# Performance work log

Hardware: AMD Instinct MI355X
Metric: run time of the kernel (lower is better)

Reference implementation:

```python
import jax, jax.numpy as jnp
import numpy as np

N, E, F, C, ED, G, D = 50000, 1000000, 30, 64, 11, 1024, 256


def setup_inputs() -> dict:
    key = jax.random.key(0)
    ks = jax.random.split(key, 20)
    rn = lambda k, shape, s=0.1: jax.random.normal(k, shape, jnp.float32) * s
    return {
        "x": rn(ks[0], (N, F), 1.0),
        "edge_attr": jax.random.uniform(ks[1], (E, ED), jnp.float32),
        "W0": rn(ks[2], (F, C)), "asrc0": rn(ks[3], (C,)), "adst0": rn(ks[4], (C,)),
        "We0": rn(ks[5], (ED, C)), "ae0": rn(ks[6], (C,)), "Wres0": rn(ks[7], (F, C)),
        "b0": jnp.zeros((C,), jnp.float32),
        "W": rn(ks[8], (3, C, C)), "asrc": rn(ks[9], (3, C)), "adst": rn(ks[10], (3, C)),
        "We": rn(ks[11], (3, ED, C)), "ae": rn(ks[12], (3, C)), "Wres": rn(ks[13], (3, C, C)),
        "b": jnp.zeros((3, C), jnp.float32),
        "Wout": rn(ks[14], (2 * C, D)), "bout": jnp.zeros((D,), jnp.float32),
        "edge_index": jax.random.randint(ks[15], (2, E), 0, N),
        "batch_index": jnp.sort(jax.random.randint(ks[16], (N,), 0, G)),
    }


def _gat(x, src, dst, edge_attr, W, asrc, adst, We, ae, Wres, b):
    """PyG GATConv (heads=1) with edge_dim and residual=True."""
    n = x.shape[0]
    h = x @ W                                   # [N, C]
    e = edge_attr @ We                          # [E, C]
    alpha = (jnp.sum(h * asrc, -1)[src]
             + jnp.sum(h * adst, -1)[dst]
             + jnp.sum(e * ae, -1))             # [E]
    alpha = jax.nn.leaky_relu(alpha, 0.2)
    m = jax.ops.segment_max(alpha, dst, num_segments=n)
    a = jnp.exp(alpha - m[dst])
    s = jax.ops.segment_sum(a, dst, num_segments=n)
    a = a / (s[dst] + 1e-16)                    # per-dst softmax
    out = jax.ops.segment_sum(a[:, None] * h[src], dst, num_segments=n)
    return out + x @ Wres + b


def reference(x, edge_attr, W0, asrc0, adst0, We0, ae0, Wres0, b0,
              W, asrc, adst, We, ae, Wres, b, Wout, bout,
              edge_index, batch_index):
    src, dst = edge_index[0], edge_index[1]
    h = jax.nn.leaky_relu(
        _gat(x, src, dst, edge_attr, W0, asrc0, adst0, We0, ae0, Wres0, b0), 0.01)
    for i in range(3):  # conv1..conv3 (fixed small layer loop)
        h = _gat(h, src, dst, edge_attr, W[i], asrc[i], adst[i],
                 We[i], ae[i], Wres[i], b[i])
        if i < 2:
            h = jax.nn.leaky_relu(h, 0.01)
    gmax = jax.ops.segment_max(h, batch_index, num_segments=G)
    gmax = jnp.where(jnp.isfinite(gmax), gmax, 0.0)  # empty graphs -> 0
    cnt = jax.ops.segment_sum(jnp.ones((h.shape[0],), h.dtype), batch_index,
                              num_segments=G)
    gmean = jax.ops.segment_sum(h, batch_index, num_segments=G) / jnp.maximum(cnt, 1.0)[:, None]
    pooled = jax.nn.leaky_relu(jnp.concatenate([gmax, gmean], axis=1), 0.01)
    return pooled @ Wout + bout
```

## Files before the change

### kernel.cpp

```cpp
#include <hip/hip_runtime.h>
#include <hip/hip_fp16.h>

#define NN 50000
#define NE 1000000
#define FIN0 30
#define C 64
#define ED 11
#define NG 1024
#define DOUT 256
#define NBIN 196
#define PA_EDGES 1024

typedef unsigned long long ull;

__global__ __launch_bounds__(256) void hist196_kernel(const int* __restrict__ dst,
    int* __restrict__ bcnt){
  __shared__ int h[256];
  int t=threadIdx.x;
  h[t]=0;
  __syncthreads();
  for(int i=blockIdx.x*256+t;i<NE;i+=gridDim.x*256)
    atomicAdd(&h[dst[i]>>8],1);
  __syncthreads();
  if(h[t]) atomicAdd(&bcnt[t],h[t]);
}

__global__ __launch_bounds__(256) void scan196_kernel(const int* __restrict__ bcnt,
    int* __restrict__ bbase, int* __restrict__ gcur){
  __shared__ int p[256];
  int t=threadIdx.x;
  int v=bcnt[t];
  p[t]=v; __syncthreads();
  #pragma unroll
  for(int off=1;off<256;off<<=1){
    int u=(t>=off)?p[t-off]:0;
    __syncthreads(); p[t]+=u; __syncthreads();
  }
  int ex=p[t]-v;
  if(t<=NBIN) bbase[t]=ex;
  if(t<NBIN)  gcur[t]=ex;
}

__global__ __launch_bounds__(256) void grow_kernel(const int* __restrict__ batch,
    int* __restrict__ growptr){
  int i=blockIdx.x*256+threadIdx.x;
  if(i>=NN) return;
  int bi=batch[i];
  int bp=(i==0)?-1:batch[i-1];
  for(int g=bp+1;g<=bi;++g) growptr[g]=i;
  if(i==NN-1){ for(int g=bi+1;g<=NG;++g) growptr[g]=NN; }
}

__global__ __launch_bounds__(256) void part_kernel(const int* __restrict__ dst,
    const int* __restrict__ src, const float* __restrict__ edge_attr,
    const float* __restrict__ We0, const float* __restrict__ ae0,
    const float* __restrict__ We,  const float* __restrict__ ae,
    int* __restrict__ gcur,
    ull* __restrict__ pdst_src, ushort4* __restrict__ ped){
  __shared__ ull     ldst_src[PA_EDGES];
  __shared__ ushort4 led[PA_EDGES];
  __shared__ unsigned char lbin[PA_EDGES];
  __shared__ float tile[256*ED];
  __shared__ float sw[4][ED];
  __shared__ int hist[256], p[256], sc[256], lofs[256], bb[256];
  int t=threadIdx.x;
  hist[t]=0;
  if(t<4*ED){
    int l=t/ED, j=t%ED;
    const float* wp=(l==0)? (We0+(size_t)j*C) : (We+((size_t)(l-1)*ED+j)*C);
    const float* ap=(l==0)? ae0 : (ae+(size_t)(l-1)*C);
    float s=0.f;
    for(int c=0;c<C;++c) s+=wp[c]*ap[c];
    sw[l][j]=s;
  }
  __syncthreads();
  size_t e0=(size_t)blockIdx.x*PA_EDGES;
  int cnt=(int)min((size_t)PA_EDGES,(size_t)NE-e0);
  for(int i=t;i<cnt;i+=256) atomicAdd(&hist[dst[e0+i]>>8],1);
  __syncthreads();
  p[t]=hist[t]; __syncthreads();
  #pragma unroll
  for(int off=1;off<256;off<<=1){
    int u=(t>=off)?p[t-off]:0;
    __syncthreads(); p[t]+=u; __syncthreads();
  }
  sc[t]=p[t]-hist[t];
  lofs[t]=sc[t];
  bb[t]=(hist[t]>0)?atomicAdd(&gcur[t],hist[t]):0;
  __syncthreads();
  for(int base=0;base<cnt;base+=256){
    int ccnt=min(256,cnt-base);
    for(int i=t;i<ccnt*ED;i+=256) tile[i]=edge_attr[(e0+base)*ED+i];
    __syncthreads();
    if(t<ccnt){
      int i=base+t;
      int d=dst[e0+i], s=src[e0+i];
      int b=d>>8;
      float d0=0,d1=0,d2=0,d3=0;
      #pragma unroll
      for(int j=0;j<ED;++j){
        float ev=tile[t*ED+j];
        d0=fmaf(ev,sw[0][j],d0);
        d1=fmaf(ev,sw[1][j],d1);
        d2=fmaf(ev,sw[2][j],d2);
        d3=fmaf(ev,sw[3][j],d3);
      }
      int slot=atomicAdd(&lofs[b],1);
      ldst_src[slot]=((ull)(unsigned)d<<32)|(unsigned)s;
      ushort4 hv;
      hv.x=__half_as_ushort(__float2half(d0));
      hv.y=__half_as_ushort(__float2half(d1));
      hv.z=__half_as_ushort(__float2half(d2));
      hv.w=__half_as_ushort(__float2half(d3));
      led[slot]=hv;
      lbin[slot]=(unsigned char)b;
    }
    __syncthreads();
  }
  for(int i=t;i<cnt;i+=256){
    int b=lbin[i];
    int g=bb[b]+i-sc[b];
    pdst_src[g]=ldst_src[i];
    ped[g]=led[i];
  }
}

__global__ __launch_bounds__(256) void build_kernel(const ull* __restrict__ pdst_src,
    const ushort4* __restrict__ ped, const int* __restrict__ bbase,
    int* __restrict__ rowptr, int* __restrict__ src_csr, ushort* __restrict__ edch){
  __shared__ int cnt[256], p[256], cur[256];
  int t=threadIdx.x, b=blockIdx.x;
  int n0=b<<8;
  cnt[t]=0;
  __syncthreads();
  int beg=bbase[b], endd=bbase[b+1];
  for(int j=beg+t;j<endd;j+=256)
    atomicAdd(&cnt[(int)(pdst_src[j]>>32)-n0],1);
  __syncthreads();
  int v=cnt[t];
  p[t]=v; __syncthreads();
  #pragma unroll
  for(int off=1;off<256;off<<=1){
    int u=(t>=off)?p[t-off]:0;
    __syncthreads(); p[t]+=u; __syncthreads();
  }
  int ex=p[t]-v;
  cur[t]=beg+ex;
  if(n0+t<NN) rowptr[n0+t]=beg+ex;
  if(b==0&&t==0) rowptr[NN]=NE;
  __syncthreads();
  for(int j=beg+t;j<endd;j+=256){
    ull ds=pdst_src[j];
    int d=(int)(ds>>32);
    int s=(int)(ds&0xffffffffu);
    int pos=atomicAdd(&cur[d-n0],1);
    src_csr[pos]=s;
    ushort4 e=ped[j];
    edch[pos]=e.x;
    edch[(size_t)NE+pos]=e.y;
    edch[2*(size_t)NE+pos]=e.z;
    edch[3*(size_t)NE+pos]=e.w;
  }
}

template<int FIN, int SXS>
__global__ __launch_bounds__(256) void feat_kernel(const float* __restrict__ in,
    const float* __restrict__ W, const float* __restrict__ Wres,
    const float* __restrict__ bvec, const float* __restrict__ av_src,
    const float* __restrict__ av_dst,
    __half* __restrict__ hW16, float* __restrict__ outb,
    float* __restrict__ as_, float* __restrict__ ad_){
  __shared__ float sW[FIN*C], sR[FIN*C];
  __shared__ float sx[64*SXS];
  __shared__ float sb[C], ss[C], sd[C];
  int tid=threadIdx.x;
  if(tid<C){ sb[tid]=bvec[tid]; ss[tid]=av_src[tid]; sd[tid]=av_dst[tid]; }
  for(int i=tid;i<FIN*C;i+=256){ sW[i]=W[i]; sR[i]=Wres[i]; }
  int nbase=blockIdx.x*64;
  int nvalid=min(64,NN-nbase);
  if constexpr (FIN==64){
    const float4* in4=(const float4*)(in+(size_t)nbase*64);
    for(int i=tid;i<1024;i+=256){
      int n=i>>4, k=(i&15)*4;
      float4 v=(n<nvalid)?in4[i]:make_float4(0.f,0.f,0.f,0.f);
      *(float4*)&sx[n*SXS+k]=v;
    }
  } else {
    for(int i=tid;i<64*FIN;i+=256){
      int n=i/FIN, k=i-n*FIN;
      sx[n*SXS+k]=(n<nvalid)?in[(size_t)(nbase+n)*FIN+k]:0.f;
    }
  }
  __syncthreads();
  int w=tid>>6, lane=tid&63;
  int ng=lane>>4, cl=lane&15;
  int n0=w*16+ng*4;
  int c0=cl*4;
  float hw[4][4]={}, hr[4][4]={};
  const float* sxp=&sx[n0*SXS];
  #pragma unroll 2
  for(int k=0;k<FIN;k+=2){
    float4 wv0=*(const float4*)&sW[k*C+c0];
    float4 rv0=*(const float4*)&sR[k*C+c0];
    float4 wv1=*(const float4*)&sW[(k+1)*C+c0];
    float4 rv1=*(const float4*)&sR[(k+1)*C+c0];
    float2 x0=*(const float2*)&sxp[k];
    float2 x1=*(const float2*)&sxp[SXS+k];
    float2 x2=*(const float2*)&sxp[2*SXS+k];
    float2 x3=*(const float2*)&sxp[3*SXS+k];
    float xa[4]={x0.x,x1.x,x2.x,x3.x};
    float xb[4]={x0.y,x1.y,x2.y,x3.y};
    #pragma unroll
    for(int r=0;r<4;++r){
      hw[r][0]=fmaf(xa[r],wv0.x,hw[r][0]);
      hw[r][1]=fmaf(xa[r],wv0.y,hw[r][1]);
      hw[r][2]=fmaf(xa[r],wv0.z,hw[r][2]);
      hw[r][3]=fmaf(xa[r],wv0.w,hw[r][3]);
      hr[r][0]=fmaf(xa[r],rv0.x,hr[r][0]);
      hr[r][1]=fmaf(xa[r],rv0.y,hr[r][1]);
      hr[r][2]=fmaf(xa[r],rv0.z,hr[r][2]);
      hr[r][3]=fmaf(xa[r],rv0.w,hr[r][3]);
      hw[r][0]=fmaf(xb[r],wv1.x,hw[r][0]);
      hw[r][1]=fmaf(xb[r],wv1.y,hw[r][1]);
      hw[r][2]=fmaf(xb[r],wv1.z,hw[r][2]);
      hw[r][3]=fmaf(xb[r],wv1.w,hw[r][3]);
      hr[r][0]=fmaf(xb[r],rv1.x,hr[r][0]);
      hr[r][1]=fmaf(xb[r],rv1.y,hr[r][1]);
      hr[r][2]=fmaf(xb[r],rv1.z,hr[r][2]);
      hr[r][3]=fmaf(xb[r],rv1.w,hr[r][3]);
    }
  }
  float s0=ss[c0], s1=ss[c0+1], s2=ss[c0+2], s3=ss[c0+3];
  float d0=sd[c0], d1=sd[c0+1], d2=sd[c0+2], d3=sd[c0+3];
  float b0v=sb[c0], b1v=sb[c0+1], b2v=sb[c0+2], b3v=sb[c0+3];
  #pragma unroll
  for(int r=0;r<4;++r){
    int n=n0+r;
    float ps=hw[r][0]*s0+hw[r][1]*s1+hw[r][2]*s2+hw[r][3]*s3;
    float pd=hw[r][0]*d0+hw[r][1]*d1+hw[r][2]*d2+hw[r][3]*d3;
    #pragma unroll
    for(int off=1;off<16;off<<=1){ ps+=__shfl_xor(ps,off,64); pd+=__shfl_xor(pd,off,64); }
    if(n<nvalid){
      size_t gn=(size_t)(nbase+n);
      ushort4 hv;
      hv.x=__half_as_ushort(__float2half(hw[r][0]));
      hv.y=__half_as_ushort(__float2half(hw[r][1]));
      hv.z=__half_as_ushort(__float2half(hw[r][2]));
      hv.w=__half_as_ushort(__float2half(hw[r][3]));
      *(ushort4*)&hW16[gn*C+c0]=hv;
      float4 ov;
      ov.x=hr[r][0]+b0v; ov.y=hr[r][1]+b1v; ov.z=hr[r][2]+b2v; ov.w=hr[r][3]+b3v;
      *(float4*)&outb[gn*C+c0]=ov;
      if(cl==0){ as_[gn]=ps; ad_[gn]=pd; }
    }
  }
}

__device__ __forceinline__ void acc8(float* a, float at, uint4 u){
  __half2 h0=*(__half2*)&u.x, h1=*(__half2*)&u.y, h2=*(__half2*)&u.z, h3=*(__half2*)&u.w;
  float2 f0=__half22float2(h0), f1=__half22float2(h1);
  float2 f2=__half22float2(h2), f3=__half22float2(h3);
  a[0]=fmaf(at,f0.x,a[0]); a[1]=fmaf(at,f0.y,a[1]);
  a[2]=fmaf(at,f1.x,a[2]); a[3]=fmaf(at,f1.y,a[3]);
  a[4]=fmaf(at,f2.x,a[4]); a[5]=fmaf(at,f2.y,a[5]);
  a[6]=fmaf(at,f3.x,a[6]); a[7]=fmaf(at,f3.y,a[7]);
}

__global__ __launch_bounds__(256) void agg_kernel(const int* __restrict__ rowptr,
    const int* __restrict__ src_csr, const ushort* __restrict__ edc_l,
    const float* __restrict__ as_, const float* __restrict__ ad_,
    const __half* __restrict__ hW16, float* __restrict__ outb, int relu){
  __shared__ float2 sws[4][64];
  int w=threadIdx.x>>6, lane=threadIdx.x&63;
  int nidx=blockIdx.x*4+w;
  if(nidx>=NN) return;
  int beg=rowptr[nidx], end=rowptr[nidx+1];
  int deg=end-beg;
  float ad_n=ad_[nidx];
  int g2=lane>>3, gl2=lane&7;
  const uint4* hw4=(const uint4*)hW16;
  float s=0.f;
  float acc[8]={0.f,0.f,0.f,0.f,0.f,0.f,0.f,0.f};

  if(deg<=64){
    int j=beg+lane;
    float al=-INFINITY; int sl=0;
    if(lane<deg){
      sl=src_csr[j];
      float a=as_[sl]+ad_n+__half2float(__ushort_as_half(edc_l[j]));
      al=(a>0.f)?a:0.2f*a;
    }
    float mn=al;
    #pragma unroll
    for(int off=32;off;off>>=1) mn=fmaxf(mn,__shfl_xor(mn,off,64));
    float wl=(lane<deg)?__expf(al-mn):0.f;
    s=wl;
    #pragma unroll
    for(int off=32;off;off>>=1) s+=__shfl_xor(s,off,64);
    float2 pr; pr.x=wl; pr.y=__int_as_float(sl);
    sws[w][lane]=pr;
    int t=g2;
    for(; t+8<deg; t+=16){
      float2 r0=sws[w][t], r1=sws[w][t+8];
      uint4 u0=hw4[(size_t)__float_as_int(r0.y)*8+gl2];
      uint4 u1=hw4[(size_t)__float_as_int(r1.y)*8+gl2];
      acc8(acc,r0.x,u0);
      acc8(acc,r1.x,u1);
    }
    if(t<deg){
      float2 r=sws[w][t];
      uint4 u=hw4[(size_t)__float_as_int(r.y)*8+gl2];
      acc8(acc,r.x,u);
    }
  } else {
    float m=-INFINITY;
    for(int base=beg;base<end;base+=64){
      int j=base+lane;
      float al=-INFINITY; int sl=0;
      if(j<end){
        sl=src_csr[j];
        float a=as_[sl]+ad_n+__half2float(__ushort_as_half(edc_l[j]));
        al=(a>0.f)?a:0.2f*a;
      }
      float cm=al;
      #pragma unroll
      for(int off=32;off;off>>=1) cm=fmaxf(cm,__shfl_xor(cm,off,64));
      float mn=fmaxf(m,cm);
      float scale=(m==-INFINITY)?0.f:__expf(m-mn);
      s*=scale;
      #pragma unroll
      for(int i=0;i<8;++i) acc[i]*=scale;
      float wl=(j<end)?__expf(al-mn):0.f;
      float cs=wl;
      #pragma unroll
      for(int off=32;off;off>>=1) cs+=__shfl_xor(cs,off,64);
      s+=cs; m=mn;
      float2 pr; pr.x=wl; pr.y=__int_as_float(sl);
      sws[w][lane]=pr;
      int cnt=min(64,end-base);
      int t=g2;
      for(; t+8<cnt; t+=16){
        float2 r0=sws[w][t], r1=sws[w][t+8];
        uint4 u0=hw4[(size_t)__float_as_int(r0.y)*8+gl2];
        uint4 u1=hw4[(size_t)__float_as_int(r1.y)*8+gl2];
        acc8(acc,r0.x,u0);
        acc8(acc,r1.x,u1);
      }
      if(t<cnt){
        float2 r=sws[w][t];
        uint4 u=hw4[(size_t)__float_as_int(r.y)*8+gl2];
        acc8(acc,r.x,u);
      }
    }
  }

  #pragma unroll
  for(int off=8;off<64;off<<=1){
    #pragma unroll
    for(int i=0;i<8;++i) acc[i]+=__shfl_xor(acc[i],off,64);
  }
  if(g2==0){
    float denom=s+1e-16f;
    size_t o0=(size_t)nidx*C+gl2*8;
    float4 oa=*(float4*)&outb[o0];
    float4 ob=*(float4*)&outb[o0+4];
    float4 va,vb;
    va.x=acc[0]/denom+oa.x; va.y=acc[1]/denom+oa.y;
    va.z=acc[2]/denom+oa.z; va.w=acc[3]/denom+oa.w;
    vb.x=acc[4]/denom+ob.x; vb.y=acc[5]/denom+ob.y;
    vb.z=acc[6]/denom+ob.z; vb.w=acc[7]/denom+ob.w;
    if(relu){
      va.x=(va.x>0.f)?va.x:0.01f*va.x; va.y=(va.y>0.f)?va.y:0.01f*va.y;
      va.z=(va.z>0.f)?va.z:0.01f*va.z; va.w=(va.w>0.f)?va.w:0.01f*va.w;
      vb.x=(vb.x>0.f)?vb.x:0.01f*vb.x; vb.y=(vb.y>0.f)?vb.y:0.01f*vb.y;
      vb.z=(vb.z>0.f)?vb.z:0.01f*vb.z; vb.w=(vb.w>0.f)?vb.w:0.01f*vb.w;
    }
    *(float4*)&outb[o0]=va;
    *(float4*)&outb[o0+4]=vb;
  }
}

__global__ __launch_bounds__(256) void pool_kernel(const float* __restrict__ h,
    const int* __restrict__ growptr, float* __restrict__ pooled){
  int w=threadIdx.x>>6, lane=threadIdx.x&63;
  int g=blockIdx.x*4+w;
  if(g>=NG) return;
  int beg=growptr[g], end=growptr[g+1];
  float mx=-INFINITY, sm=0.f;
  for(int n=beg;n<end;++n){ float v=h[(size_t)n*C+lane]; mx=fmaxf(mx,v); sm+=v; }
  int cnt=end-beg;
  float gm=(cnt==0)?0.f:mx;
  float mean=sm/fmaxf((float)cnt,1.f);
  gm=(gm>0.f)?gm:0.01f*gm;
  mean=(mean>0.f)?mean:0.01f*mean;
  pooled[(size_t)g*128+lane]=gm;
  pooled[(size_t)g*128+64+lane]=mean;
}

__global__ __launch_bounds__(256) void out_kernel(const float* __restrict__ pooled,
    const float* __restrict__ Wout, const float* __restrict__ bout,
    float* __restrict__ out){
  __shared__ float sp[128];
  int g=blockIdx.x, d=threadIdx.x;
  if(d<128) sp[d]=pooled[(size_t)g*128+d];
  __syncthreads();
  float o=bout[d];
  for(int k=0;k<128;++k) o=fmaf(sp[k],Wout[k*DOUT+d],o);
  out[(size_t)g*DOUT+d]=o;
}

extern "C" void kernel_launch(void* const* d_in, const int* in_sizes, int n_in,
                              void* d_out, int out_size, void* d_ws, size_t ws_size,
                              hipStream_t stream){
  const float* x        =(const float*)d_in[0];
  const float* edge_attr=(const float*)d_in[1];
  const float* W0       =(const float*)d_in[2];
  const float* asrc0    =(const float*)d_in[3];
  const float* adst0    =(const float*)d_in[4];
  const float* We0      =(const float*)d_in[5];
  const float* ae0      =(const float*)d_in[6];
  const float* Wres0    =(const float*)d_in[7];
  const float* b0       =(const float*)d_in[8];
  const float* W        =(const float*)d_in[9];
  const float* asrc     =(const float*)d_in[10];
  const float* adst     =(const float*)d_in[11];
  const float* We       =(const float*)d_in[12];
  const float* ae       =(const float*)d_in[13];
  const float* Wres     =(const float*)d_in[14];
  const float* b        =(const float*)d_in[15];
  const float* Wout     =(const float*)d_in[16];
  const float* bout     =(const float*)d_in[17];
  const int* edge_index =(const int*)d_in[18];
  const int* batch_index=(const int*)d_in[19];
  const int* src=edge_index;
  const int* dst=edge_index+NE;

  char* p=(char*)d_ws;
  auto take=[&](size_t bytes)->void*{ void* r=(void*)p; p+=(bytes+255)&~(size_t)255; return r; };
  int* rowptr  =(int*)take((size_t)(NN+1)*4);
  int* growptr =(int*)take((size_t)(NG+1)*4);
  int* bcnt    =(int*)take((size_t)256*4);
  int* bbase   =(int*)take((size_t)256*4);
  int* gcur    =(int*)take((size_t)256*4);
  int* src_csr =(int*)take((size_t)NE*4);
  float* as_   =(float*)take((size_t)NN*4);
  float* ad_   =(float*)take((size_t)NN*4);
  ushort* edch =(ushort*)take((size_t)NE*4*2);
  __half* hW16 =(__half*)take((size_t)NN*C*2);
  float* bufA  =(float*)take((size_t)NN*C*4);
  ull* pdst_src=(ull*)take((size_t)NE*8);
  float* pooled=(float*)pdst_src;
  ushort4* ped =(ushort4*)take((size_t)NN*C*4);
  float* bufB  =(float*)ped;
  (void)ws_size; (void)in_sizes; (void)n_in; (void)out_size;

  hipMemsetAsync(bcnt,0,(size_t)256*4,stream);
  hist196_kernel<<<1024,256,0,stream>>>(dst,bcnt);
  scan196_kernel<<<1,256,0,stream>>>(bcnt,bbase,gcur);
  grow_kernel<<<(NN+255)/256,256,0,stream>>>(batch_index,growptr);

  part_kernel<<<(NE+PA_EDGES-1)/PA_EDGES,256,0,stream>>>(dst,src,edge_attr,
      We0,ae0,We,ae,gcur,pdst_src,ped);
  build_kernel<<<NBIN,256,0,stream>>>(pdst_src,ped,bbase,rowptr,src_csr,edch);

  const int nblkF=(NN+63)/64;
  const int nblkA=(NN+3)/4;
  feat_kernel<FIN0,36><<<nblkF,256,0,stream>>>(x,W0,Wres0,b0,asrc0,adst0,hW16,bufA,as_,ad_);
  agg_kernel<<<nblkA,256,0,stream>>>(rowptr,src_csr,edch,as_,ad_,hW16,bufA,1);
  float* bin=bufA; float* bo=bufB;
  for(int i=0;i<3;++i){
    feat_kernel<C,68><<<nblkF,256,0,stream>>>(bin,W+(size_t)i*C*C,Wres+(size_t)i*C*C,
        b+(size_t)i*C,asrc+(size_t)i*C,adst+(size_t)i*C,hW16,bo,as_,ad_);
    agg_kernel<<<nblkA,256,0,stream>>>(rowptr,src_csr,edch+(size_t)(i+1)*NE,as_,ad_,hW16,bo,(i<2)?1:0);
    float* t=bin; bin=bo; bo=t;
  }
  pool_kernel<<<(NG+3)/4,256,0,stream>>>(bin,growptr,pooled);
  out_kernel<<<NG,256,0,stream>>>(pooled,Wout,bout,(float*)d_out);
}
```

Before: 338.2 us.

## Process two nodes per wavefront in aggregation and pack partition records into uint4

The aggregation kernel now assigns two destination nodes per 64-lane wavefront, one per 32-lane half, when every degree in the wave is at most 32. Waves with a larger degree fall back to a sequential per-node loop. This targets idle lanes, since the average degree is about 20 and many lanes sat unused. The partition step also merges the dst/src and half-precision edge-score arrays into one 16-byte record and doubles the edges per partition block, giving fewer, wider stores and loads. The grid size NN/8 relies on NN being divisible by 8, and the fallback path serialises the two nodes.

```diff
diff --git a/kernel.cpp b/kernel.cpp
--- a/kernel.cpp
+++ b/kernel.cpp
@@ -9,7 +9,7 @@
 #define NG 1024
 #define DOUT 256
 #define NBIN 196
-#define PA_EDGES 1024
+#define PA_EDGES 2048
 
 typedef unsigned long long ull;
 
@@ -55,10 +55,8 @@
     const int* __restrict__ src, const float* __restrict__ edge_attr,
     const float* __restrict__ We0, const float* __restrict__ ae0,
     const float* __restrict__ We,  const float* __restrict__ ae,
-    int* __restrict__ gcur,
-    ull* __restrict__ pdst_src, ushort4* __restrict__ ped){
-  __shared__ ull     ldst_src[PA_EDGES];
-  __shared__ ushort4 led[PA_EDGES];
+    int* __restrict__ gcur, uint4* __restrict__ prec){
+  __shared__ uint4 lrec[PA_EDGES];
   __shared__ unsigned char lbin[PA_EDGES];
   __shared__ float tile[256*ED];
   __shared__ float sw[4][ED];
@@ -105,14 +103,14 @@
         d2=fmaf(ev,sw[2][j],d2);
         d3=fmaf(ev,sw[3][j],d3);
       }
+      uint4 r;
+      r.x=(unsigned)d; r.y=(unsigned)s;
+      r.z=(unsigned)__half_as_ushort(__float2half(d0))
+         |((unsigned)__half_as_ushort(__float2half(d1))<<16);
+      r.w=(unsigned)__half_as_ushort(__float2half(d2))
+         |((unsigned)__half_as_ushort(__float2half(d3))<<16);
       int slot=atomicAdd(&lofs[b],1);
-      ldst_src[slot]=((ull)(unsigned)d<<32)|(unsigned)s;
-      ushort4 hv;
-      hv.x=__half_as_ushort(__float2half(d0));
-      hv.y=__half_as_ushort(__float2half(d1));
-      hv.z=__half_as_ushort(__float2half(d2));
-      hv.w=__half_as_ushort(__float2half(d3));
-      led[slot]=hv;
+      lrec[slot]=r;
       lbin[slot]=(unsigned char)b;
     }
     __syncthreads();
@@ -120,13 +118,12 @@
   for(int i=t;i<cnt;i+=256){
     int b=lbin[i];
     int g=bb[b]+i-sc[b];
-    pdst_src[g]=ldst_src[i];
-    ped[g]=led[i];
-  }
-}
-
-__global__ __launch_bounds__(256) void build_kernel(const ull* __restrict__ pdst_src,
-    const ushort4* __restrict__ ped, const int* __restrict__ bbase,
+    prec[g]=lrec[i];
+  }
+}
+
+__global__ __launch_bounds__(256) void build_kernel(const uint4* __restrict__ prec,
+    const int* __restrict__ bbase,
     int* __restrict__ rowptr, int* __restrict__ src_csr, ushort* __restrict__ edch){
   __shared__ int cnt[256], p[256], cur[256];
   int t=threadIdx.x, b=blockIdx.x;
@@ -135,7 +132,7 @@
   __syncthreads();
   int beg=bbase[b], endd=bbase[b+1];
   for(int j=beg+t;j<endd;j+=256)
-    atomicAdd(&cnt[(int)(pdst_src[j]>>32)-n0],1);
+    atomicAdd(&cnt[(int)prec[j].x-n0],1);
   __syncthreads();
   int v=cnt[t];
   p[t]=v; __syncthreads();
@@ -150,16 +147,14 @@
   if(b==0&&t==0) rowptr[NN]=NE;
   __syncthreads();
   for(int j=beg+t;j<endd;j+=256){
-    ull ds=pdst_src[j];
-    int d=(int)(ds>>32);
-    int s=(int)(ds&0xffffffffu);
+    uint4 r=prec[j];
+    int d=(int)r.x, s=(int)r.y;
     int pos=atomicAdd(&cur[d-n0],1);
     src_csr[pos]=s;
-    ushort4 e=ped[j];
-    edch[pos]=e.x;
-    edch[(size_t)NE+pos]=e.y;
-    edch[2*(size_t)NE+pos]=e.z;
-    edch[3*(size_t)NE+pos]=e.w;
+    edch[pos]                =(ushort)(r.z&0xffffu);
+    edch[(size_t)NE+pos]     =(ushort)(r.z>>16);
+    edch[2*(size_t)NE+pos]   =(ushort)(r.w&0xffffu);
+    edch[3*(size_t)NE+pos]   =(ushort)(r.w>>16);
   }
 }
 
@@ -272,111 +267,177 @@
     const __half* __restrict__ hW16, float* __restrict__ outb, int relu){
   __shared__ float2 sws[4][64];
   int w=threadIdx.x>>6, lane=threadIdx.x&63;
-  int nidx=blockIdx.x*4+w;
-  if(nidx>=NN) return;
+  int half=lane>>5, hl=lane&31;
+  int n0=blockIdx.x*8+w*2;
+  int nidx=n0+half;
   int beg=rowptr[nidx], end=rowptr[nidx+1];
   int deg=end-beg;
-  float ad_n=ad_[nidx];
-  int g2=lane>>3, gl2=lane&7;
   const uint4* hw4=(const uint4*)hW16;
-  float s=0.f;
-  float acc[8]={0.f,0.f,0.f,0.f,0.f,0.f,0.f,0.f};
-
-  if(deg<=64){
-    int j=beg+lane;
+
+  if(__all(deg<=32)){
+    float ad_n=ad_[nidx];
+    int j=beg+hl;
     float al=-INFINITY; int sl=0;
-    if(lane<deg){
+    if(hl<deg){
       sl=src_csr[j];
       float a=as_[sl]+ad_n+__half2float(__ushort_as_half(edc_l[j]));
       al=(a>0.f)?a:0.2f*a;
     }
     float mn=al;
     #pragma unroll
-    for(int off=32;off;off>>=1) mn=fmaxf(mn,__shfl_xor(mn,off,64));
-    float wl=(lane<deg)?__expf(al-mn):0.f;
-    s=wl;
+    for(int off=16;off;off>>=1) mn=fmaxf(mn,__shfl_xor(mn,off,64));
+    float wl=(hl<deg)?__expf(al-mn):0.f;
+    float s=wl;
     #pragma unroll
-    for(int off=32;off;off>>=1) s+=__shfl_xor(s,off,64);
+    for(int off=16;off;off>>=1) s+=__shfl_xor(s,off,64);
     float2 pr; pr.x=wl; pr.y=__int_as_float(sl);
     sws[w][lane]=pr;
-    int t=g2;
-    for(; t+8<deg; t+=16){
-      float2 r0=sws[w][t], r1=sws[w][t+8];
-      uint4 u0=hw4[(size_t)__float_as_int(r0.y)*8+gl2];
-      uint4 u1=hw4[(size_t)__float_as_int(r1.y)*8+gl2];
+    int g=hl>>3, gl=hl&7;
+    float acc[8]={0.f,0.f,0.f,0.f,0.f,0.f,0.f,0.f};
+    int base=half*32;
+    int t=g;
+    for(; t+4<deg; t+=8){
+      float2 r0=sws[w][base+t], r1=sws[w][base+t+4];
+      uint4 u0=hw4[(size_t)__float_as_int(r0.y)*8+gl];
+      uint4 u1=hw4[(size_t)__float_as_int(r1.y)*8+gl];
       acc8(acc,r0.x,u0);
       acc8(acc,r1.x,u1);
     }
     if(t<deg){
-      float2 r=sws[w][t];
-      uint4 u=hw4[(size_t)__float_as_int(r.y)*8+gl2];
+      float2 r=sws[w][base+t];
+      uint4 u=hw4[(size_t)__float_as_int(r.y)*8+gl];
       acc8(acc,r.x,u);
     }
-  } else {
-    float m=-INFINITY;
-    for(int base=beg;base<end;base+=64){
-      int j=base+lane;
+    #pragma unroll
+    for(int off=8;off<=16;off<<=1){
+      #pragma unroll
+      for(int i=0;i<8;++i) acc[i]+=__shfl_xor(acc[i],off,64);
+    }
+    if(hl<8){
+      float denom=s+1e-16f;
+      size_t o0=(size_t)nidx*C+hl*8;
+      float4 oa=*(float4*)&outb[o0];
+      float4 ob=*(float4*)&outb[o0+4];
+      float4 va,vb;
+      va.x=acc[0]/denom+oa.x; va.y=acc[1]/denom+oa.y;
+      va.z=acc[2]/denom+oa.z; va.w=acc[3]/denom+oa.w;
+      vb.x=acc[4]/denom+ob.x; vb.y=acc[5]/denom+ob.y;
+      vb.z=acc[6]/denom+ob.z; vb.w=acc[7]/denom+ob.w;
+      if(relu){
+        va.x=(va.x>0.f)?va.x:0.01f*va.x; va.y=(va.y>0.f)?va.y:0.01f*va.y;
+        va.z=(va.z>0.f)?va.z:0.01f*va.z; va.w=(va.w>0.f)?va.w:0.01f*va.w;
+        vb.x=(vb.x>0.f)?vb.x:0.01f*vb.x; vb.y=(vb.y>0.f)?vb.y:0.01f*vb.y;
+        vb.z=(vb.z>0.f)?vb.z:0.01f*vb.z; vb.w=(vb.w>0.f)?vb.w:0.01f*vb.w;
+      }
+      *(float4*)&outb[o0]=va;
+      *(float4*)&outb[o0+4]=vb;
+    }
+    return;
+  }
+
+  for(int h=0;h<2;++h){
+    int m=n0+h;
+    int bh=__shfl(beg,h*32,64);
+    int dh=__shfl(deg,h*32,64);
+    float ad_n=ad_[m];
+    int g2=lane>>3, gl2=lane&7;
+    float s=0.f;
+    float acc[8]={0.f,0.f,0.f,0.f,0.f,0.f,0.f,0.f};
+    if(dh<=64){
+      int j=bh+lane;
       float al=-INFINITY; int sl=0;
-      if(j<end){
+      if(lane<dh){
         sl=src_csr[j];
         float a=as_[sl]+ad_n+__half2float(__ushort_as_half(edc_l[j]));
         al=(a>0.f)?a:0.2f*a;
       }
-      float cm=al;
+      float mn=al;
       #pragma unroll
-      for(int off=32;off;off>>=1) cm=fmaxf(cm,__shfl_xor(cm,off,64));
-      float mn=fmaxf(m,cm);
-      float scale=(m==-INFINITY)?0.f:__expf(m-mn);
-      s*=scale;
+      for(int off=32;off;off>>=1) mn=fmaxf(mn,__shfl_xor(mn,off,64));
+      float wl=(lane<dh)?__expf(al-mn):0.f;
+      s=wl;
       #pragma unroll
-      for(int i=0;i<8;++i) acc[i]*=scale;
-      float wl=(j<end)?__expf(al-mn):0.f;
-      float cs=wl;
-      #pragma unroll
-      for(int off=32;off;off>>=1) cs+=__shfl_xor(cs,off,64);
-      s+=cs; m=mn;
+      for(int off=32;off;off>>=1) s+=__shfl_xor(s,off,64);
       float2 pr; pr.x=wl; pr.y=__int_as_float(sl);
       sws[w][lane]=pr;
-      int cnt=min(64,end-base);
       int t=g2;
-      for(; t+8<cnt; t+=16){
+      for(; t+8<dh; t+=16){
         float2 r0=sws[w][t], r1=sws[w][t+8];
         uint4 u0=hw4[(size_t)__float_as_int(r0.y)*8+gl2];
         uint4 u1=hw4[(size_t)__float_as_int(r1.y)*8+gl2];
         acc8(acc,r0.x,u0);
         acc8(acc,r1.x,u1);
       }
-      if(t<cnt){
+      if(t<dh){
         float2 r=sws[w][t];
         uint4 u=hw4[(size_t)__float_as_int(r.y)*8+gl2];
         acc8(acc,r.x,u);
       }
-    }
-  }
-
-  #pragma unroll
-  for(int off=8;off<64;off<<=1){
+    } else {
+      float m_=-INFINITY;
+      for(int base=bh;base<bh+dh;base+=64){
+        int j=base+lane;
+        float al=-INFINITY; int sl=0;
+        if(j<bh+dh){
+          sl=src_csr[j];
+          float a=as_[sl]+ad_n+__half2float(__ushort_as_half(edc_l[j]));
+          al=(a>0.f)?a:0.2f*a;
+        }
+        float cm=al;
+        #pragma unroll
+        for(int off=32;off;off>>=1) cm=fmaxf(cm,__shfl_xor(cm,off,64));
+        float mn=fmaxf(m_,cm);
+        float scale=(m_==-INFINITY)?0.f:__expf(m_-mn);
+        s*=scale;
+        #pragma unroll
+        for(int i=0;i<8;++i) acc[i]*=scale;
+        float wl=(j<bh+dh)?__expf(al-mn):0.f;
+        float cs=wl;
+        #pragma unroll
+        for(int off=32;off;off>>=1) cs+=__shfl_xor(cs,off,64);
+        s+=cs; m_=mn;
+        float2 pr; pr.x=wl; pr.y=__int_as_float(sl);
+        sws[w][lane]=pr;
+        int cnt=min(64,bh+dh-base);
+        int t=g2;
+        for(; t+8<cnt; t+=16){
+          float2 r0=sws[w][t], r1=sws[w][t+8];
+          uint4 u0=hw4[(size_t)__float_as_int(r0.y)*8+gl2];
+          uint4 u1=hw4[(size_t)__float_as_int(r1.y)*8+gl2];
+          acc8(acc,r0.x,u0);
+          acc8(acc,r1.x,u1);
+        }
+        if(t<cnt){
+          float2 r=sws[w][t];
+          uint4 u=hw4[(size_t)__float_as_int(r.y)*8+gl2];
+          acc8(acc,r.x,u);
+        }
+      }
+    }
     #pragma unroll
-    for(int i=0;i<8;++i) acc[i]+=__shfl_xor(acc[i],off,64);
-  }
-  if(g2==0){
-    float denom=s+1e-16f;
-    size_t o0=(size_t)nidx*C+gl2*8;
-    float4 oa=*(float4*)&outb[o0];
-    float4 ob=*(float4*)&outb[o0+4];
-    float4 va,vb;
-    va.x=acc[0]/denom+oa.x; va.y=acc[1]/denom+oa.y;
-    va.z=acc[2]/denom+oa.z; va.w=acc[3]/denom+oa.w;
-    vb.x=acc[4]/denom+ob.x; vb.y=acc[5]/denom+ob.y;
-    vb.z=acc[6]/denom+ob.z; vb.w=acc[7]/denom+ob.w;
-    if(relu){
-      va.x=(va.x>0.f)?va.x:0.01f*va.x; va.y=(va.y>0.f)?va.y:0.01f*va.y;
-      va.z=(va.z>0.f)?va.z:0.01f*va.z; va.w=(va.w>0.f)?va.w:0.01f*va.w;
-      vb.x=(vb.x>0.f)?vb.x:0.01f*vb.x; vb.y=(vb.y>0.f)?vb.y:0.01f*vb.y;
-      vb.z=(vb.z>0.f)?vb.z:0.01f*vb.z; vb.w=(vb.w>0.f)?vb.w:0.01f*vb.w;
-    }
-    *(float4*)&outb[o0]=va;
-    *(float4*)&outb[o0+4]=vb;
+    for(int off=8;off<64;off<<=1){
+      #pragma unroll
+      for(int i=0;i<8;++i) acc[i]+=__shfl_xor(acc[i],off,64);
+    }
+    if(g2==0){
+      float denom=s+1e-16f;
+      size_t o0=(size_t)m*C+gl2*8;
+      float4 oa=*(float4*)&outb[o0];
+      float4 ob=*(float4*)&outb[o0+4];
+      float4 va,vb;
+      va.x=acc[0]/denom+oa.x; va.y=acc[1]/denom+oa.y;
+      va.z=acc[2]/denom+oa.z; va.w=acc[3]/denom+oa.w;
+      vb.x=acc[4]/denom+ob.x; vb.y=acc[5]/denom+ob.y;
+      vb.z=acc[6]/denom+ob.z; vb.w=acc[7]/denom+ob.w;
+      if(relu){
+        va.x=(va.x>0.f)?va.x:0.01f*va.x; va.y=(va.y>0.f)?va.y:0.01f*va.y;
+        va.z=(va.z>0.f)?va.z:0.01f*va.z; va.w=(va.w>0.f)?va.w:0.01f*va.w;
+        vb.x=(vb.x>0.f)?vb.x:0.01f*vb.x; vb.y=(vb.y>0.f)?vb.y:0.01f*vb.y;
+        vb.z=(vb.z>0.f)?vb.z:0.01f*vb.z; vb.w=(vb.w>0.f)?vb.w:0.01f*vb.w;
+      }
+      *(float4*)&outb[o0]=va;
+      *(float4*)&outb[o0+4]=vb;
+    }
   }
 }
 
@@ -448,10 +509,9 @@
   ushort* edch =(ushort*)take((size_t)NE*4*2);
   __half* hW16 =(__half*)take((size_t)NN*C*2);
   float* bufA  =(float*)take((size_t)NN*C*4);
-  ull* pdst_src=(ull*)take((size_t)NE*8);
-  float* pooled=(float*)pdst_src;
-  ushort4* ped =(ushort4*)take((size_t)NN*C*4);
-  float* bufB  =(float*)ped;
+  uint4* prec  =(uint4*)take((size_t)NE*16);
+  float* bufB  =(float*)prec;
+  float* pooled=(float*)take((size_t)NG*128*4);
   (void)ws_size; (void)in_sizes; (void)n_in; (void)out_size;
 
   hipMemsetAsync(bcnt,0,(size_t)256*4,stream);
@@ -460,11 +520,11 @@
   grow_kernel<<<(NN+255)/256,256,0,stream>>>(batch_index,growptr);
 
   part_kernel<<<(NE+PA_EDGES-1)/PA_EDGES,256,0,stream>>>(dst,src,edge_attr,
-      We0,ae0,We,ae,gcur,pdst_src,ped);
-  build_kernel<<<NBIN,256,0,stream>>>(pdst_src,ped,bbase,rowptr,src_csr,edch);
+      We0,ae0,We,ae,gcur,prec);
+  build_kernel<<<NBIN,256,0,stream>>>(prec,bbase,rowptr,src_csr,edch);
 
   const int nblkF=(NN+63)/64;
-  const int nblkA=(NN+3)/4;
+  const int nblkA=NN/8;
   feat_kernel<FIN0,36><<<nblkF,256,0,stream>>>(x,W0,Wres0,b0,asrc0,adst0,hW16,bufA,as_,ad_);
   agg_kernel<<<nblkA,256,0,stream>>>(rowptr,src_csr,edch,as_,ad_,hW16,bufA,1);
   float* bin=bufA; float* bo=bufB;
```

Measured after the change: 312.5 us. -7.6%, faster.
